# Kernel optimization log

Measured on AMD Instinct MI355X. Metric: run time of the kernel, lower is better.

## Reference

```python
import jax, jax.numpy as jnp
import numpy as np

EPS = 1e-5
GROUPS = 8

def group_norm(x, gamma, beta):
    # x: [B,C,H,W], 8 groups
    B, C, H, W = x.shape
    xg = x.reshape(B, GROUPS, C // GROUPS, H, W)
    mu = jnp.mean(xg, axis=(2, 3, 4), keepdims=True)
    var = jnp.mean((xg - mu) ** 2, axis=(2, 3, 4), keepdims=True)
    xn = ((xg - mu) * jax.lax.rsqrt(var + EPS)).reshape(B, C, H, W)
    return xn * gamma[None, :, None, None] + beta[None, :, None, None]

def setup_inputs() -> dict:
    key = jax.random.key(0)
    ks = jax.random.split(key, 7)
    B, C, H, W = 4, 256, 64, 64
    x = jax.random.normal(ks[0], (B, C, H, W), dtype=jnp.float32)
    gamma = jnp.ones((C,), dtype=jnp.float32)
    beta = jnp.zeros((C,), dtype=jnp.float32)
    s = 1.0 / np.sqrt(C)
    w_qkv = jax.random.normal(ks[1], (3 * C, C), dtype=jnp.float32) * s
    b_qkv = jnp.zeros((3 * C,), dtype=jnp.float32)
    w_proj = jax.random.normal(ks[2], (C, C), dtype=jnp.float32) * s
    b_proj = jnp.zeros((C,), dtype=jnp.float32)
    return {"x": x, "gamma": gamma, "beta": beta, "w_qkv": w_qkv,
            "b_qkv": b_qkv, "w_proj": w_proj, "b_proj": b_proj}

def reference(x, gamma, beta, w_qkv, b_qkv, w_proj, b_proj):
    B, C, H, W = x.shape
    N = H * W
    h = group_norm(x, gamma, beta)
    # 1x1 conv == per-pixel matmul
    qkv = jnp.einsum('bchw,oc->bohw', h, w_qkv) + b_qkv[None, :, None, None]
    q, k, v = jnp.split(qkv, 3, axis=1)  # each [B,C,H,W]
    q = q.reshape(B, C, N).transpose(0, 2, 1)   # [B,N,C]
    k = k.reshape(B, C, N)                      # [B,C,N]
    v = v.reshape(B, C, N).transpose(0, 2, 1)   # [B,N,C]
    attn = jax.nn.softmax(jnp.einsum('bnc,bcm->bnm', q, k) / jnp.sqrt(jnp.float32(C)), axis=-1)
    out = jnp.einsum('bnm,bmc->bnc', attn, v)   # [B,N,C]
    out = out.transpose(0, 2, 1).reshape(B, C, H, W)
    proj = jnp.einsum('bchw,oc->bohw', out, w_proj) + b_proj[None, :, None, None]
    return x + proj
```

## Files before the change

### kernel.cpp

```cpp
#include <hip/hip_runtime.h>
#include <hip/hip_bf16.h>
#include <math.h>

#define B 4
#define C 256
#define G 8
#define N 4096
#define EPSV 1e-5f
#define SCALE 0.0625f

typedef __attribute__((ext_vector_type(8))) short short8;
typedef __attribute__((ext_vector_type(16))) float f32x16;
typedef unsigned short ushort_t;
typedef unsigned int uint_t;

__device__ __forceinline__ ushort_t f2bf(float f) {
    union { float f; uint_t u; } c; c.f = f;
    uint_t u = c.u;
    uint_t r = (u + 0x7FFFu + ((u >> 16) & 1u)) >> 16;
    return (ushort_t)r;
}
__device__ __forceinline__ float bf2f(ushort_t h) {
    union { uint_t u; float f; } c; c.u = ((uint_t)h) << 16;
    return c.f;
}
__device__ __forceinline__ uint_t pack2(float a, float b) {
    return (uint_t)f2bf(a) | ((uint_t)f2bf(b) << 16);
}
__device__ __forceinline__ uint_t cvtpk_bf16(float lo, float hi) {
    uint_t r;
    asm("v_cvt_pk_bf16_f32 %0, %1, %2" : "=v"(r) : "v"(lo), "v"(hi));
    return r;
}
__device__ __forceinline__ void gl_lds16(const void* g, void* l) {
    __builtin_amdgcn_global_load_lds(
        (const __attribute__((address_space(1))) void*)g,
        (__attribute__((address_space(3))) void*)l, 16, 0, 0);
}

__global__ __launch_bounds__(256) void gn_wconv(const float* __restrict__ x,
        float* __restrict__ partials, const float* __restrict__ wq,
        const float* __restrict__ wp, ushort_t* __restrict__ wbf) {
    int blk = blockIdx.x;
    if (blk < 256) {
        int bg = blk >> 3;
        int part = blk & 7;
        const float4* xp4 = (const float4*)(x + (size_t)bg * (32 * N) + (size_t)part * (32 * N / 8));
        float s = 0.f, ss = 0.f;
        for (int i = threadIdx.x; i < 4096; i += 256) {
            float4 v = xp4[i];
            s  += v.x + v.y + v.z + v.w;
            ss += v.x*v.x + v.y*v.y + v.z*v.z + v.w*v.w;
        }
        __shared__ float rs[256], rss[256];
        rs[threadIdx.x] = s; rss[threadIdx.x] = ss;
        __syncthreads();
        for (int off = 128; off > 0; off >>= 1) {
            if (threadIdx.x < off) {
                rs[threadIdx.x]  += rs[threadIdx.x + off];
                rss[threadIdx.x] += rss[threadIdx.x + off];
            }
            __syncthreads();
        }
        if (threadIdx.x == 0) {
            partials[(bg*8 + part)*2]     = rs[0];
            partials[(bg*8 + part)*2 + 1] = rss[0];
        }
    } else {
        int idx = (blk - 256)*256 + threadIdx.x;
        #pragma unroll
        for (int p = 0; p < 4; p++) {
            int id = idx + p*16384;
            float4 v = (id < 49152) ? ((const float4*)wq)[id] : ((const float4*)wp)[id - 49152];
            uint2 pk; pk.x = pack2(v.x, v.y); pk.y = pack2(v.z, v.w);
            *(uint2*)&wbf[(size_t)id*4] = pk;
        }
    }
}

__global__ void gn_final(const float* __restrict__ partials, float* __restrict__ stats) {
    int t = threadIdx.x;
    if (t < 32) {
        float s = 0.f, ss = 0.f;
        for (int p = 0; p < 8; p++) {
            s  += partials[(t*8 + p)*2];
            ss += partials[(t*8 + p)*2 + 1];
        }
        const float inv = 1.f / 131072.f;
        float mu = s * inv;
        float var = fmaxf(ss * inv - mu*mu, 0.f);
        stats[t*2]     = mu;
        stats[t*2 + 1] = rsqrtf(var + EPSV);
    }
}

__global__ __launch_bounds__(256) void qkv_fused(const float* __restrict__ x,
        const ushort_t* __restrict__ wbf, const float* __restrict__ gamma,
        const float* __restrict__ beta, const float* __restrict__ stats,
        const float* __restrict__ bias,
        ushort_t* __restrict__ qbf, ushort_t* __restrict__ kimg, ushort_t* __restrict__ vimg) {
    int b = blockIdx.z, o0 = blockIdx.y*128, n0 = blockIdx.x*128;
    int tid = threadIdx.x;
    int w = tid>>6, l = tid&63, l31 = l&31, lh = l>>5;
    int cg = tid >> 5;
    int nq = tid & 31;
    __shared__ short Ws[2][8192];
    __shared__ short Hs[2][8192];

    const ushort_t* wb = wbf + (size_t)o0*256;

    auto stageW = [&](int bb, int c0) {
        #pragma unroll
        for (int q = 0; q < 4; q++) {
            int u0 = (q*4 + w)*64;
            int u  = u0 + l;
            int row = u & 127, ch = u >> 7;
            gl_lds16(wb + (size_t)row*256 + c0 + ch*8, &Ws[bb][u0*8]);
        }
    };
    auto loadX = [&](int c0, float4* xv) {
        const float* xb = x + ((size_t)b*C + c0 + cg*8)*N + n0 + nq*4;
        #pragma unroll
        for (int e = 0; e < 8; e++)
            xv[e] = *(const float4*)(xb + (size_t)e*N);
    };
    auto writeH = [&](int bb, int c0, const float4* xv) {
        int cbase = c0 + cg*8;
        int g = cbase >> 5;
        float mu = stats[(b*G+g)*2], rs = stats[(b*G+g)*2+1];
        float ga[8], be[8];
        #pragma unroll
        for (int e = 0; e < 8; e++) {
            float gm = gamma[cbase+e];
            ga[e] = gm*rs;
            be[e] = beta[cbase+e] - mu*ga[e];
        }
        #pragma unroll
        for (int j = 0; j < 4; j++) {
            float h[8];
            #pragma unroll
            for (int e = 0; e < 8; e++) {
                float vx = (j==0) ? xv[e].x : (j==1) ? xv[e].y : (j==2) ? xv[e].z : xv[e].w;
                h[e] = vx*ga[e] + be[e];
            }
            uint4 pk;
            pk.x = pack2(h[0], h[1]);
            pk.y = pack2(h[2], h[3]);
            pk.z = pack2(h[4], h[5]);
            pk.w = pack2(h[6], h[7]);
            *(uint4*)&Hs[bb][(size_t)(cg*128 + nq*4 + j)*8] = pk;
        }
    };

    f32x16 acc[4];
    #pragma unroll
    for (int nf = 0; nf < 4; nf++)
        #pragma unroll
        for (int r = 0; r < 16; r++) acc[nf][r] = 0.f;

    float4 xv[8];
    loadX(0, xv);
    stageW(0, 0);
    writeH(0, 0, xv);
    __syncthreads();

    for (int t = 0; t < 4; t++) {
        int bb = t & 1;
        if (t < 3) { stageW(bb^1, (t+1)*64); loadX((t+1)*64, xv); }
        short8 af[4];
        #pragma unroll
        for (int s = 0; s < 4; s++)
            af[s] = *(const short8*)&Ws[bb][((2*s+lh)*128 + w*32 + l31)*8];
        #pragma unroll
        for (int nf = 0; nf < 4; nf++) {
            #pragma unroll
            for (int s = 0; s < 4; s++) {
                short8 hf = *(const short8*)&Hs[bb][((2*s+lh)*128 + nf*32 + l31)*8];
                acc[nf] = __builtin_amdgcn_mfma_f32_32x32x16_bf16(af[s], hf, acc[nf], 0, 0, 0);
            }
        }
        if (t < 3) writeH(bb^1, (t+1)*64, xv);
        __syncthreads();
    }

    int ow = o0 + w*32;
    float bv[16];
    #pragma unroll
    for (int r = 0; r < 16; r++) bv[r] = bias[ow + (r&3) + 8*(r>>2) + 4*lh];

    if (ow < 256) {
        #pragma unroll
        for (int nf = 0; nf < 4; nf++) {
            int n = n0 + nf*32 + l31;
            ushort_t* row = qbf + ((size_t)(b*N + n))*256 + ow;
            #pragma unroll
            for (int rp = 0; rp < 8; rp++) {
                int r0 = rp*2;
                int cl = (r0&3) + 8*(r0>>2) + 4*lh;
                uint_t wd = cvtpk_bf16((acc[nf][r0]+bv[r0])*SCALE, (acc[nf][r0+1]+bv[r0+1])*SCALE);
                *(uint_t*)(row + cl) = wd;
            }
        }
    } else if (ow < 512) {
        int cb = ow - 256;
        #pragma unroll
        for (int nf = 0; nf < 4; nf++) {
            int n = n0 + nf*32 + l31;
            ushort_t* tbase = kimg + (size_t)b*1048576 + (size_t)(n>>5)*8192
                            + (size_t)l31*8 + 4*lh;
            #pragma unroll
            for (int g = 0; g < 4; g++) {
                uint2 pk;
                pk.x = pack2(acc[nf][g*4+0]+bv[g*4+0], acc[nf][g*4+1]+bv[g*4+1]);
                pk.y = pack2(acc[nf][g*4+2]+bv[g*4+2], acc[nf][g*4+3]+bv[g*4+3]);
                *(uint2*)(tbase + (size_t)((cb>>3)+g)*256) = pk;
            }
        }
    } else {
        int cb = ow - 512;
        #pragma unroll
        for (int nf = 0; nf < 4; nf++) {
            int n = n0 + nf*32 + l31;
            ushort_t* tbase = vimg + (size_t)b*1048576 + (size_t)(n>>5)*8192
                            + (size_t)(l31>>3)*2048 + (l31&7);
            #pragma unroll
            for (int r = 0; r < 16; r++) {
                int cl = (r&3) + 8*(r>>2) + 4*lh;
                tbase[(size_t)(cb+cl)*8] = f2bf(acc[nf][r] + bv[r]);
            }
        }
    }
}

__global__ __launch_bounds__(256, 2) void attn_mfma(const ushort_t* __restrict__ qbf,
        const ushort_t* __restrict__ kimg, const ushort_t* __restrict__ vimg,
        ushort_t* __restrict__ part, float* __restrict__ ml) {
    int f = blockIdx.x;
    int comb = f & 15;
    int qt  = f >> 4;
    int b   = comb >> 2;
    int kvq = comb & 3;
    constexpr int NT = 32;
    int w = threadIdx.x >> 6;
    int l = threadIdx.x & 63;
    int l31 = l & 31, lh = l >> 5;

    __shared__ short KV[2][2][8192];

    int qbase = qt*128 + w*32;
    short8 qf[16];
    {
        const ushort_t* qrow = qbf + ((size_t)(b*N + qbase + l31))*256;
        #pragma unroll
        for (int s = 0; s < 16; s++)
            qf[s] = *(const short8*)(qrow + s*16 + lh*8);
    }

    f32x16 ot[8];
    #pragma unroll
    for (int mc = 0; mc < 8; mc++)
        #pragma unroll
        for (int r = 0; r < 16; r++) ot[mc][r] = 0.f;
    float m = -INFINITY, lsum = 0.f;

    const char* kbase = (const char*)kimg + (size_t)b*2097152;
    const char* vbase = (const char*)vimg + (size_t)b*2097152;

    auto stage = [&](int slot, int t) {
        int tile = kvq*32 + t;
        const char* kt = kbase + (size_t)tile*16384;
        const char* vt = vbase + (size_t)tile*16384;
        #pragma unroll
        for (int q = 0; q < 4; q++) {
            int u0 = (w*4 + q)*64;
            gl_lds16(kt + (u0 + l)*16, &KV[slot][0][u0*8]);
            gl_lds16(vt + (u0 + l)*16, &KV[slot][1][u0*8]);
        }
    };

    stage(0, 0);

    for (int t = 0; t < NT; t++) {
        int slot = t & 1;
        __syncthreads();
        if (t+1 < NT) stage(slot^1, t+1);

        f32x16 st0, st1;
        #pragma unroll
        for (int r = 0; r < 16; r++) { st0[r] = 0.f; st1[r] = 0.f; }
        const short* kb_ = &KV[slot][0][0];
        __builtin_amdgcn_s_setprio(1);
        #pragma unroll
        for (int s = 0; s < 8; s++) {
            short8 ka = *(const short8*)(kb_ + ((size_t)((4*s   + lh)*32 + l31))*8);
            short8 kc = *(const short8*)(kb_ + ((size_t)((4*s+2 + lh)*32 + l31))*8);
            st0 = __builtin_amdgcn_mfma_f32_32x32x16_bf16(ka, qf[2*s],   st0, 0, 0, 0);
            st1 = __builtin_amdgcn_mfma_f32_32x32x16_bf16(kc, qf[2*s+1], st1, 0, 0, 0);
        }
        __builtin_amdgcn_s_setprio(0);

        float sv[16];
        #pragma unroll
        for (int r = 0; r < 16; r++) sv[r] = st0[r] + st1[r];
        float pmax = sv[0];
        #pragma unroll
        for (int r = 1; r < 16; r++) pmax = fmaxf(pmax, sv[r]);
        pmax = fmaxf(pmax, __shfl_xor(pmax, 32));
        if (!__all(pmax <= m + 8.0f)) {
            float mn = fmaxf(m, pmax);
            float fac = __expf(m - mn);
            m = mn;
            lsum *= fac;
            #pragma unroll
            for (int mc = 0; mc < 8; mc++)
                #pragma unroll
                for (int r = 0; r < 16; r++) ot[mc][r] *= fac;
        }
        float p[16]; float ls = 0.f;
        #pragma unroll
        for (int r = 0; r < 16; r++) { p[r] = __expf(sv[r] - m); ls += p[r]; }
        ls += __shfl_xor(ls, 32);
        lsum += ls;

        short8 pf0, pf1;
        {
            uint_t x0 = cvtpk_bf16(p[0], p[1]);
            uint_t y0 = cvtpk_bf16(p[4], p[5]);
            uint_t x1 = cvtpk_bf16(p[2], p[3]);
            uint_t y1 = cvtpk_bf16(p[6], p[7]);
            auto r0 = __builtin_amdgcn_permlane32_swap(x0, y0, false, false);
            auto r1 = __builtin_amdgcn_permlane32_swap(x1, y1, false, false);
            union { uint_t u[4]; short8 s8; } u_;
            u_.u[0] = r0[0]; u_.u[1] = r1[0]; u_.u[2] = r0[1]; u_.u[3] = r1[1];
            pf0 = u_.s8;
            uint_t x2 = cvtpk_bf16(p[8],  p[9]);
            uint_t y2 = cvtpk_bf16(p[12], p[13]);
            uint_t x3 = cvtpk_bf16(p[10], p[11]);
            uint_t y3 = cvtpk_bf16(p[14], p[15]);
            auto r2 = __builtin_amdgcn_permlane32_swap(x2, y2, false, false);
            auto r3 = __builtin_amdgcn_permlane32_swap(x3, y3, false, false);
            union { uint_t u[4]; short8 s8; } u2_;
            u2_.u[0] = r2[0]; u2_.u[1] = r3[0]; u2_.u[2] = r2[1]; u2_.u[3] = r3[1];
            pf1 = u2_.s8;
        }

        const short* vb_ = &KV[slot][1][0];
        __builtin_amdgcn_s_setprio(1);
        #pragma unroll
        for (int mc = 0; mc < 8; mc++) {
            short8 v0 = *(const short8*)(vb_ + ((size_t)((lh)*256   + mc*32 + l31))*8);
            short8 v1 = *(const short8*)(vb_ + ((size_t)((2+lh)*256 + mc*32 + l31))*8);
            ot[mc] = __builtin_amdgcn_mfma_f32_32x32x16_bf16(v0, pf0, ot[mc], 0, 0, 0);
            ot[mc] = __builtin_amdgcn_mfma_f32_32x32x16_bf16(v1, pf1, ot[mc], 0, 0, 0);
        }
        __builtin_amdgcn_s_setprio(0);
    }

    float invl = 1.f / lsum;
    ushort_t* pbase = part + (size_t)kvq*4194304 + ((size_t)(b*N + qbase + l31))*256;
    #pragma unroll
    for (int mc = 0; mc < 8; mc++)
        #pragma unroll
        for (int rp = 0; rp < 8; rp++) {
            int r0 = rp*2;
            uint_t wd = cvtpk_bf16(ot[mc][r0]*invl, ot[mc][r0+1]*invl);
            int c0 = (r0 & 3) + 8*(r0 >> 2) + 4*lh + 32*mc;
            *(uint_t*)(pbase + c0) = wd;
        }
    if (l < 32) {
        size_t row = (size_t)kvq*16384 + b*4096 + qbase + l;
        ml[row*2]     = m;
        ml[row*2 + 1] = lsum;
    }
}

template<int NS>
__global__ __launch_bounds__(256) void attn_merge(const ushort_t* __restrict__ part,
        const float* __restrict__ ml, ushort_t* __restrict__ ob) {
    int t = blockIdx.x*256 + threadIdx.x;
    int row = t >> 5;
    int c8 = (t & 31) * 8;
    float mv[NS], lv[NS];
    float M = -INFINITY;
    #pragma unroll
    for (int i = 0; i < NS; i++) {
        mv[i] = ml[((size_t)i*16384 + row)*2];
        lv[i] = ml[((size_t)i*16384 + row)*2 + 1];
        M = fmaxf(M, mv[i]);
    }
    float wv[NS]; float wsum = 0.f;
    #pragma unroll
    for (int i = 0; i < NS; i++) { wv[i] = __expf(mv[i] - M)*lv[i]; wsum += wv[i]; }
    float inv = 1.f / wsum;
    float o[8];
    #pragma unroll
    for (int e = 0; e < 8; e++) o[e] = 0.f;
    #pragma unroll
    for (int i = 0; i < NS; i++) {
        const ushort_t* p = part + (size_t)i*4194304 + (size_t)row*256 + c8;
        float wi = wv[i]*inv;
        #pragma unroll
        for (int e = 0; e < 8; e++) o[e] += wi*bf2f(p[e]);
    }
    uint4 pk;
    pk.x = pack2(o[0], o[1]);
    pk.y = pack2(o[2], o[3]);
    pk.z = pack2(o[4], o[5]);
    pk.w = pack2(o[6], o[7]);
    *(uint4*)(ob + (size_t)row*256 + c8) = pk;
}

__global__ __launch_bounds__(256) void proj_mfma(const ushort_t* __restrict__ obf,
        const ushort_t* __restrict__ wpbf, const float* __restrict__ bp,
        const float* __restrict__ x, float* __restrict__ out) {
    int b = blockIdx.z, o0 = blockIdx.y*128, n0 = blockIdx.x*64;
    int tid = threadIdx.x;
    int w = tid>>6, l = tid&63, l31 = l&31, lh = l>>5;
    __shared__ short Ws[2][8192];
    __shared__ short Hs[2][4096];

    const ushort_t* wb = wpbf + (size_t)o0*256;
    const ushort_t* hb = obf + ((size_t)b*N + n0)*256;

    auto stage = [&](int bb, int c0) {
        #pragma unroll
        for (int q = 0; q < 4; q++) {
            int u0 = (q*4 + w)*64;
            int u  = u0 + l;
            int row = u & 127, ch = u >> 7;
            gl_lds16(wb + (size_t)row*256 + c0 + ch*8, &Ws[bb][u0*8]);
        }
        #pragma unroll
        for (int q = 0; q < 2; q++) {
            int u0 = (q*4 + w)*64;
            int u  = u0 + l;
            int row = u & 63, ch = u >> 6;
            gl_lds16(hb + (size_t)row*256 + c0 + ch*8, &Hs[bb][u0*8]);
        }
    };

    f32x16 acc[2];
    #pragma unroll
    for (int nf = 0; nf < 2; nf++)
        #pragma unroll
        for (int r = 0; r < 16; r++) acc[nf][r] = 0.f;

    stage(0, 0);
    __syncthreads();
    for (int t = 0; t < 4; t++) {
        int bb = t & 1;
        if (t < 3) stage(bb^1, (t+1)*64);
        short8 af[4];
        #pragma unroll
        for (int s = 0; s < 4; s++)
            af[s] = *(const short8*)&Ws[bb][((2*s+lh)*128 + w*32 + l31)*8];
        #pragma unroll
        for (int nf = 0; nf < 2; nf++) {
            #pragma unroll
            for (int s = 0; s < 4; s++) {
                short8 hf = *(const short8*)&Hs[bb][((2*s+lh)*64 + nf*32 + l31)*8];
                acc[nf] = __builtin_amdgcn_mfma_f32_32x32x16_bf16(af[s], hf, acc[nf], 0, 0, 0);
            }
        }
        __syncthreads();
    }

    int cw = o0 + w*32;
    float bv[16];
    #pragma unroll
    for (int r = 0; r < 16; r++) bv[r] = bp[cw + (r&3) + 8*(r>>2) + 4*lh];

    #pragma unroll
    for (int nf = 0; nf < 2; nf++) {
        int n = n0 + nf*32 + l31;
        #pragma unroll
        for (int r = 0; r < 16; r++) {
            int cl = (r&3) + 8*(r>>2) + 4*lh;
            size_t a = ((size_t)b*C + cw + cl)*N + n;
            out[a] = acc[nf][r] + bv[r] + x[a];
        }
    }
}

extern "C" void kernel_launch(void* const* d_in, const int* in_sizes, int n_in,
                              void* d_out, int out_size, void* d_ws, size_t ws_size,
                              hipStream_t stream) {
    const float* x      = (const float*)d_in[0];
    const float* gamma  = (const float*)d_in[1];
    const float* beta   = (const float*)d_in[2];
    const float* w_qkv  = (const float*)d_in[3];
    const float* b_qkv  = (const float*)d_in[4];
    const float* w_proj = (const float*)d_in[5];
    const float* b_proj = (const float*)d_in[6];
    float* out = (float*)d_out;
    char* wsb  = (char*)d_ws;

    const size_t MB = 1048576;
    ushort_t* qbf  = (ushort_t*)(wsb);
    ushort_t* kimg = (ushort_t*)(wsb + 8*MB);
    ushort_t* vimg = (ushort_t*)(wsb + 16*MB);
    ushort_t* part = (ushort_t*)(wsb + 24*MB);
    float*    ml   = (float*)  (wsb + 56*MB);
    ushort_t* ob   = (ushort_t*)(wsb + 56*MB + 524288);
    float* partials = (float*) (wsb + 64*MB + 524288);
    float* stats    = partials + 512;
    ushort_t* wbf  = (ushort_t*)(wsb + 64*MB + 524288 + 4096);

    gn_wconv<<<dim3(320), dim3(256), 0, stream>>>(x, partials, w_qkv, w_proj, wbf);
    gn_final<<<dim3(1), dim3(64), 0, stream>>>(partials, stats);
    qkv_fused<<<dim3(32, 6, 4), dim3(256), 0, stream>>>(x, wbf, gamma, beta, stats, b_qkv, qbf, kimg, vimg);
    attn_mfma<<<dim3(512), dim3(256), 0, stream>>>(qbf, kimg, vimg, part, ml);
    attn_merge<4><<<dim3(2048), dim3(256), 0, stream>>>(part, ml, ob);
    proj_mfma<<<dim3(64, 2, 4), dim3(256), 0, stream>>>(ob, wbf + 196608, b_proj, x, out);
}
```

Before: 137.2 us.

## Fuse GN finalize into QKV, merge into projection, and use exp2 softmax

Drops the gn_final launch by having each qkv_fused block reduce its batch's group partials into shared memory. Drops the separate attn_merge kernel by merging the split-K attention partials inside the projection GEMM's H staging. The log2(e) factor is folded into the Q scale so the softmax uses exp2f, with the rescale threshold adjusted to match, and the max and sum reductions become trees. The aim is fewer launches and no round trip through the merged output buffer, at the cost of redundant stat and merge work per block and merge loads that are not asynchronous.

```diff
diff --git a/kernel.cpp b/kernel.cpp
--- a/kernel.cpp
+++ b/kernel.cpp
@@ -7,7 +7,8 @@
 #define G 8
 #define N 4096
 #define EPSV 1e-5f
-#define SCALE 0.0625f
+#define QSCALE 0.0901684400f
+#define THR2 11.5416f
 
 typedef __attribute__((ext_vector_type(8))) short short8;
 typedef __attribute__((ext_vector_type(16))) float f32x16;
@@ -78,25 +79,9 @@
     }
 }
 
-__global__ void gn_final(const float* __restrict__ partials, float* __restrict__ stats) {
-    int t = threadIdx.x;
-    if (t < 32) {
-        float s = 0.f, ss = 0.f;
-        for (int p = 0; p < 8; p++) {
-            s  += partials[(t*8 + p)*2];
-            ss += partials[(t*8 + p)*2 + 1];
-        }
-        const float inv = 1.f / 131072.f;
-        float mu = s * inv;
-        float var = fmaxf(ss * inv - mu*mu, 0.f);
-        stats[t*2]     = mu;
-        stats[t*2 + 1] = rsqrtf(var + EPSV);
-    }
-}
-
 __global__ __launch_bounds__(256) void qkv_fused(const float* __restrict__ x,
         const ushort_t* __restrict__ wbf, const float* __restrict__ gamma,
-        const float* __restrict__ beta, const float* __restrict__ stats,
+        const float* __restrict__ beta, const float* __restrict__ partials,
         const float* __restrict__ bias,
         ushort_t* __restrict__ qbf, ushort_t* __restrict__ kimg, ushort_t* __restrict__ vimg) {
     int b = blockIdx.z, o0 = blockIdx.y*128, n0 = blockIdx.x*128;
@@ -106,6 +91,22 @@
     int nq = tid & 31;
     __shared__ short Ws[2][8192];
     __shared__ short Hs[2][8192];
+    __shared__ float sst[16];
+
+    if (tid < 8) {
+        float s = 0.f, ss = 0.f;
+        #pragma unroll
+        for (int p = 0; p < 8; p++) {
+            s  += partials[((b*8 + tid)*8 + p)*2];
+            ss += partials[((b*8 + tid)*8 + p)*2 + 1];
+        }
+        const float inv = 1.f / 131072.f;
+        float mu = s * inv;
+        float var = fmaxf(ss * inv - mu*mu, 0.f);
+        sst[tid*2]     = mu;
+        sst[tid*2 + 1] = rsqrtf(var + EPSV);
+    }
+    __syncthreads();
 
     const ushort_t* wb = wbf + (size_t)o0*256;
 
@@ -127,7 +128,7 @@
     auto writeH = [&](int bb, int c0, const float4* xv) {
         int cbase = c0 + cg*8;
         int g = cbase >> 5;
-        float mu = stats[(b*G+g)*2], rs = stats[(b*G+g)*2+1];
+        float mu = sst[g*2], rs = sst[g*2+1];
         float ga[8], be[8];
         #pragma unroll
         for (int e = 0; e < 8; e++) {
@@ -197,7 +198,7 @@
             for (int rp = 0; rp < 8; rp++) {
                 int r0 = rp*2;
                 int cl = (r0&3) + 8*(r0>>2) + 4*lh;
-                uint_t wd = cvtpk_bf16((acc[nf][r0]+bv[r0])*SCALE, (acc[nf][r0+1]+bv[r0+1])*SCALE);
+                uint_t wd = cvtpk_bf16((acc[nf][r0]+bv[r0])*QSCALE, (acc[nf][r0+1]+bv[r0+1])*QSCALE);
                 *(uint_t*)(row + cl) = wd;
             }
         }
@@ -302,13 +303,17 @@
         float sv[16];
         #pragma unroll
         for (int r = 0; r < 16; r++) sv[r] = st0[r] + st1[r];
-        float pmax = sv[0];
-        #pragma unroll
-        for (int r = 1; r < 16; r++) pmax = fmaxf(pmax, sv[r]);
+
+        float a0 = fmaxf(sv[0], sv[1]),  a1 = fmaxf(sv[2], sv[3]);
+        float a2 = fmaxf(sv[4], sv[5]),  a3 = fmaxf(sv[6], sv[7]);
+        float a4 = fmaxf(sv[8], sv[9]),  a5 = fmaxf(sv[10], sv[11]);
+        float a6 = fmaxf(sv[12], sv[13]), a7 = fmaxf(sv[14], sv[15]);
+        float b0 = fmaxf(a0, a1), b1 = fmaxf(a2, a3), b2 = fmaxf(a4, a5), b3 = fmaxf(a6, a7);
+        float pmax = fmaxf(fmaxf(b0, b1), fmaxf(b2, b3));
         pmax = fmaxf(pmax, __shfl_xor(pmax, 32));
-        if (!__all(pmax <= m + 8.0f)) {
+        if (!__all(pmax <= m + THR2)) {
             float mn = fmaxf(m, pmax);
-            float fac = __expf(m - mn);
+            float fac = exp2f(m - mn);
             m = mn;
             lsum *= fac;
             #pragma unroll
@@ -316,9 +321,14 @@
                 #pragma unroll
                 for (int r = 0; r < 16; r++) ot[mc][r] *= fac;
         }
-        float p[16]; float ls = 0.f;
-        #pragma unroll
-        for (int r = 0; r < 16; r++) { p[r] = __expf(sv[r] - m); ls += p[r]; }
+        float p[16];
+        #pragma unroll
+        for (int r = 0; r < 16; r++) p[r] = exp2f(sv[r] - m);
+        float s0_ = (p[0]+p[1]) + (p[2]+p[3]);
+        float s1_ = (p[4]+p[5]) + (p[6]+p[7]);
+        float s2_ = (p[8]+p[9]) + (p[10]+p[11]);
+        float s3_ = (p[12]+p[13]) + (p[14]+p[15]);
+        float ls = (s0_+s1_) + (s2_+s3_);
         ls += __shfl_xor(ls, 32);
         lsum += ls;
 
@@ -374,45 +384,9 @@
     }
 }
 
-template<int NS>
-__global__ __launch_bounds__(256) void attn_merge(const ushort_t* __restrict__ part,
-        const float* __restrict__ ml, ushort_t* __restrict__ ob) {
-    int t = blockIdx.x*256 + threadIdx.x;
-    int row = t >> 5;
-    int c8 = (t & 31) * 8;
-    float mv[NS], lv[NS];
-    float M = -INFINITY;
-    #pragma unroll
-    for (int i = 0; i < NS; i++) {
-        mv[i] = ml[((size_t)i*16384 + row)*2];
-        lv[i] = ml[((size_t)i*16384 + row)*2 + 1];
-        M = fmaxf(M, mv[i]);
-    }
-    float wv[NS]; float wsum = 0.f;
-    #pragma unroll
-    for (int i = 0; i < NS; i++) { wv[i] = __expf(mv[i] - M)*lv[i]; wsum += wv[i]; }
-    float inv = 1.f / wsum;
-    float o[8];
-    #pragma unroll
-    for (int e = 0; e < 8; e++) o[e] = 0.f;
-    #pragma unroll
-    for (int i = 0; i < NS; i++) {
-        const ushort_t* p = part + (size_t)i*4194304 + (size_t)row*256 + c8;
-        float wi = wv[i]*inv;
-        #pragma unroll
-        for (int e = 0; e < 8; e++) o[e] += wi*bf2f(p[e]);
-    }
-    uint4 pk;
-    pk.x = pack2(o[0], o[1]);
-    pk.y = pack2(o[2], o[3]);
-    pk.z = pack2(o[4], o[5]);
-    pk.w = pack2(o[6], o[7]);
-    *(uint4*)(ob + (size_t)row*256 + c8) = pk;
-}
-
-__global__ __launch_bounds__(256) void proj_mfma(const ushort_t* __restrict__ obf,
-        const ushort_t* __restrict__ wpbf, const float* __restrict__ bp,
-        const float* __restrict__ x, float* __restrict__ out) {
+__global__ __launch_bounds__(256) void proj_merge(const ushort_t* __restrict__ part,
+        const float* __restrict__ ml, const ushort_t* __restrict__ wpbf,
+        const float* __restrict__ bp, const float* __restrict__ x, float* __restrict__ out) {
     int b = blockIdx.z, o0 = blockIdx.y*128, n0 = blockIdx.x*64;
     int tid = threadIdx.x;
     int w = tid>>6, l = tid&63, l31 = l&31, lh = l>>5;
@@ -420,9 +394,29 @@
     __shared__ short Hs[2][4096];
 
     const ushort_t* wb = wpbf + (size_t)o0*256;
-    const ushort_t* hb = obf + ((size_t)b*N + n0)*256;
-
-    auto stage = [&](int bb, int c0) {
+
+    int srow = tid & 63;
+    int ch0  = tid >> 6;
+    size_t rowbase = ((size_t)(b*4096 + n0 + srow))*256;
+    float wv[4];
+    {
+        float mv[4], lv[4];
+        #pragma unroll
+        for (int i = 0; i < 4; i++) {
+            size_t rr = (size_t)i*16384 + b*4096 + n0 + srow;
+            mv[i] = ml[rr*2];
+            lv[i] = ml[rr*2 + 1];
+        }
+        float M = fmaxf(fmaxf(mv[0], mv[1]), fmaxf(mv[2], mv[3]));
+        float wsum = 0.f;
+        #pragma unroll
+        for (int i = 0; i < 4; i++) { wv[i] = exp2f(mv[i] - M)*lv[i]; wsum += wv[i]; }
+        float inv = 1.f / wsum;
+        #pragma unroll
+        for (int i = 0; i < 4; i++) wv[i] *= inv;
+    }
+
+    auto stageW = [&](int bb, int c0) {
         #pragma unroll
         for (int q = 0; q < 4; q++) {
             int u0 = (q*4 + w)*64;
@@ -430,13 +424,36 @@
             int row = u & 127, ch = u >> 7;
             gl_lds16(wb + (size_t)row*256 + c0 + ch*8, &Ws[bb][u0*8]);
         }
-        #pragma unroll
-        for (int q = 0; q < 2; q++) {
-            int u0 = (q*4 + w)*64;
-            int u  = u0 + l;
-            int row = u & 63, ch = u >> 6;
-            gl_lds16(hb + (size_t)row*256 + c0 + ch*8, &Hs[bb][u0*8]);
-        }
+    };
+    short8 hA[4], hB[4];
+    auto Hload = [&](int c0) {
+        #pragma unroll
+        for (int i = 0; i < 4; i++) {
+            const ushort_t* pp = part + (size_t)i*4194304 + rowbase + c0;
+            hA[i] = *(const short8*)(pp + ch0*8);
+            hB[i] = *(const short8*)(pp + (ch0+4)*8);
+        }
+    };
+    auto Hwrite = [&](int bb) {
+        float oA[8], oB[8];
+        #pragma unroll
+        for (int e = 0; e < 8; e++) { oA[e] = 0.f; oB[e] = 0.f; }
+        #pragma unroll
+        for (int i = 0; i < 4; i++) {
+            float wi = wv[i];
+            #pragma unroll
+            for (int e = 0; e < 8; e++) {
+                oA[e] += wi*bf2f((ushort_t)hA[i][e]);
+                oB[e] += wi*bf2f((ushort_t)hB[i][e]);
+            }
+        }
+        uint4 pkA, pkB;
+        pkA.x = pack2(oA[0], oA[1]); pkA.y = pack2(oA[2], oA[3]);
+        pkA.z = pack2(oA[4], oA[5]); pkA.w = pack2(oA[6], oA[7]);
+        pkB.x = pack2(oB[0], oB[1]); pkB.y = pack2(oB[2], oB[3]);
+        pkB.z = pack2(oB[4], oB[5]); pkB.w = pack2(oB[6], oB[7]);
+        *(uint4*)&Hs[bb][(size_t)(ch0*64 + srow)*8]     = pkA;
+        *(uint4*)&Hs[bb][(size_t)((ch0+4)*64 + srow)*8] = pkB;
     };
 
     f32x16 acc[2];
@@ -445,11 +462,13 @@
         #pragma unroll
         for (int r = 0; r < 16; r++) acc[nf][r] = 0.f;
 
-    stage(0, 0);
+    stageW(0, 0);
+    Hload(0);
+    Hwrite(0);
     __syncthreads();
     for (int t = 0; t < 4; t++) {
         int bb = t & 1;
-        if (t < 3) stage(bb^1, (t+1)*64);
+        if (t < 3) { stageW(bb^1, (t+1)*64); Hload((t+1)*64); }
         short8 af[4];
         #pragma unroll
         for (int s = 0; s < 4; s++)
@@ -462,6 +481,7 @@
                 acc[nf] = __builtin_amdgcn_mfma_f32_32x32x16_bf16(af[s], hf, acc[nf], 0, 0, 0);
             }
         }
+        if (t < 3) Hwrite(bb^1);
         __syncthreads();
     }
 
@@ -501,15 +521,11 @@
     ushort_t* vimg = (ushort_t*)(wsb + 16*MB);
     ushort_t* part = (ushort_t*)(wsb + 24*MB);
     float*    ml   = (float*)  (wsb + 56*MB);
-    ushort_t* ob   = (ushort_t*)(wsb + 56*MB + 524288);
-    float* partials = (float*) (wsb + 64*MB + 524288);
-    float* stats    = partials + 512;
-    ushort_t* wbf  = (ushort_t*)(wsb + 64*MB + 524288 + 4096);
+    float* partials = (float*) (wsb + 56*MB + 524288);
+    ushort_t* wbf  = (ushort_t*)(wsb + 56*MB + 528384);
 
     gn_wconv<<<dim3(320), dim3(256), 0, stream>>>(x, partials, w_qkv, w_proj, wbf);
-    gn_final<<<dim3(1), dim3(64), 0, stream>>>(partials, stats);
-    qkv_fused<<<dim3(32, 6, 4), dim3(256), 0, stream>>>(x, wbf, gamma, beta, stats, b_qkv, qbf, kimg, vimg);
+    qkv_fused<<<dim3(32, 6, 4), dim3(256), 0, stream>>>(x, wbf, gamma, beta, partials, b_qkv, qbf, kimg, vimg);
     attn_mfma<<<dim3(512), dim3(256), 0, stream>>>(qbf, kimg, vimg, part, ml);
-    attn_merge<4><<<dim3(2048), dim3(256), 0, stream>>>(part, ml, ob);
-    proj_mfma<<<dim3(64, 2, 4), dim3(256), 0, stream>>>(ob, wbf + 196608, b_proj, x, out);
-}
+    proj_merge<<<dim3(64, 2, 4), dim3(256), 0, stream>>>(part, ml, wbf + 196608, b_proj, x, out);
+}
```

After: 146.9 us. 7.0% more time.
